# Kernel optimization log

Measured on AMD Instinct MI355X. Metric: run time of the kernel, lower is better.

## Reference

```python
import jax, jax.numpy as jnp
import numpy as np

H = 4096      # hidden_size
NH = 32       # num_heads
QR = 1536     # q_lora_rank
KVR = 512     # kv_lora_rank
RD = 64       # qk_rope_head_dim
ND = 128      # qk_nope_head_dim
VD = 128      # v_head_dim
QK = RD + ND  # qk_head_dim
EPS = 1e-6
THETA = 10000.0
B, S = 2, 1024


def rmsnorm(x, w):
    # torch: x / (||x|| * d^-0.5 + eps) * w
    norm = jnp.sqrt(jnp.sum(x * x, axis=-1, keepdims=True)) * (x.shape[-1] ** -0.5)
    return x / (norm + EPS) * w


def rope_cos_sin(seq_len):
    inv_freq = 1.0 / (THETA ** (jnp.arange(0, RD, 2, dtype=jnp.float32) / RD))
    t = jnp.arange(seq_len, dtype=jnp.float32)
    freqs = jnp.outer(t, inv_freq)              # [S, RD/2]
    emb = jnp.concatenate([freqs, freqs], -1)   # [S, RD]
    return jnp.cos(emb), jnpp_cos_sin_dummy() if False else jnp.sin(emb)


def rotate_half(x):
    x1, x2 = jnp.split(x, 2, axis=-1)
    return jnp.concatenate([-x2, x1], axis=-1)


def setup_inputs() -> dict:
    key = jax.random.key(0)
    ks = jax.random.split(key, 8)
    sc = 0.02
    return {
        "hidden_states": jax.random.normal(ks[0], (B, S, H), jnp.float32),
        "w_qa": jax.random.normal(ks[1], (H, QR), jnp.float32) * sc,
        "g_qa": jnp.ones((QR,), jnp.float32),
        "w_qb": jax.random.normal(ks[2], (QR, NH * QK), jnp.float32) * sc,
        "w_kva": jax.random.normal(ks[3], (H, KVR + RD), jnp.float32) * sc,
        "g_kva": jnp.ones((KVR,), jnp.float32),
        "w_kvb": jax.random.normal(ks[4], (KVR, NH * (ND + VD)), jnp.float32) * sc,
        "w_o": jax.random.normal(ks[5], (NH * VD, H), jnp.float32) * sc,
    }


def reference(hidden_states, w_qa, g_qa, w_qb, w_kva, g_kva, w_kvb, w_o):
    b, s, _ = hidden_states.shape
    # Q path: LoRA down -> RMSNorm -> LoRA up
    q_c = rmsnorm(hidden_states @ w_qa, g_qa)                       # [b,s,QR]
    q = (q_c @ w_qb).reshape(b, s, NH, QK).transpose(0, 2, 1, 3)    # [b,NH,s,QK]
    q_nope, q_rope = q[..., :ND], q[..., ND:]
    # KV path: joint down-proj, split compressed kv and rope key
    kv = hidden_states @ w_kva                                      # [b,s,KVR+RD]
    k_c, k_rope = kv[..., :KVR], kv[..., KVR:]
    k_c = rmsnorm(k_c, g_kva)
    kst = (k_c @ w_kvb).reshape(b, s, NH, ND + VD).transpose(0, 2, 1, 3)
    k_nope, v = kst[..., :ND], kst[..., ND:]                        # [b,NH,s,ND],[b,NH,s,VD]
    # partial RoPE on the rope slice only
    inv_freq = 1.0 / (THETA ** (jnp.arange(0, RD, 2, dtype=jnp.float32) / RD))
    freqs = jnp.outer(jnp.arange(s, dtype=jnp.float32), inv_freq)
    emb = jnp.concatenate([freqs, freqs], -1)                       # [s,RD]
    cos = jnp.cos(emb)[None, None]                                  # [1,1,s,RD]
    sin = jnp.sin(emb)[None, None]
    k_rope = k_rope[:, None]                                        # [b,1,s,RD]
    q_rope = q_rope * cos + rotate_half(q_rope) * sin
    k_rope = k_rope * cos + rotate_half(k_rope) * sin
    k_rope = jnp.broadcast_to(k_rope, (b, NH, s, RD))
    query = jnp.concatenate([q_nope, q_rope], -1)                   # [b,NH,s,QK]
    key_s = jnp.concatenate([k_nope, k_rope], -1)
    scaling = QK ** -0.5
    scores = jnp.einsum("bhqd,bhkd->bhqk", query, key_s) * scaling  # [b,NH,s,s]
    attn = jax.nn.softmax(scores, axis=-1)
    out = jnp.einsum("bhqk,bhkd->bhqd", attn, v)                    # [b,NH,s,VD]
    out = out.transpose(0, 2, 1, 3).reshape(b, s, NH * VD)
    return out @ w_o                                                # [b,s,H]
```

## Files before the change

### kernel.cpp

```cpp
#include <hip/hip_runtime.h>
#include <hip/hip_bf16.h>
#include <stdint.h>

typedef float f32x4_t __attribute__((ext_vector_type(4)));
typedef short s16x8_t __attribute__((ext_vector_type(8)));

#define LDS_AS __attribute__((address_space(3)))
#define GLB_AS __attribute__((address_space(1)))

__device__ __forceinline__ void gload16(void* lds, const void* g) {
    __builtin_amdgcn_global_load_lds((const GLB_AS uint32_t*)g,
                                     (LDS_AS uint32_t*)lds, 16, 0, 0);
}

__device__ __forceinline__ uint32_t pack_bf16(float lo, float hi) {
    union { __hip_bfloat16 h; uint16_t u; } a, b;
    a.h = __float2bfloat16(lo); b.h = __float2bfloat16(hi);
    return (uint32_t)a.u | ((uint32_t)b.u << 16);
}

__global__ __launch_bounds__(256) void rope_table_kernel(float* __restrict__ cos_t,
                                                         float* __restrict__ sin_t) {
    int idx = blockIdx.x * 256 + threadIdx.x;
    int s = idx >> 6, j = idx & 63;
    float invf = powf(10000.0f, -((float)((j & 31) * 2)) / 64.0f);
    float a = (float)s * invf;
    cos_t[idx] = cosf(a);
    sin_t[idx] = sinf(a);
}

__global__ __launch_bounds__(256) void f32_to_bf16_kernel(const float* __restrict__ in,
                                                          __hip_bfloat16* __restrict__ out, int n4) {
    int i = blockIdx.x * 256 + threadIdx.x;
    if (i >= n4) return;
    float4 v = reinterpret_cast<const float4*>(in)[i];
    struct __align__(8) BF4 { __hip_bfloat16 a, b, c, d; } r;
    r.a = __float2bfloat16(v.x); r.b = __float2bfloat16(v.y);
    r.c = __float2bfloat16(v.z); r.d = __float2bfloat16(v.w);
    reinterpret_cast<BF4*>(out)[i] = r;
}

__global__ __launch_bounds__(256) void transpose_convert(const float* __restrict__ W,
                                                         __hip_bfloat16* __restrict__ WT,
                                                         int K, int N, int Npad, float scale) {
    __shared__ float tile[32][132];
    int k0 = blockIdx.y * 32, n0 = blockIdx.x * 128;
    int tx = threadIdx.x & 31, ty = threadIdx.x >> 5;
#pragma unroll
    for (int i = 0; i < 4; i++) {
        int ky = i * 8 + ty;
        int n = n0 + tx * 4;
        float4 v;
        if (n + 3 < N) {
            v = *(const float4*)&W[(size_t)(k0 + ky) * N + n];
        } else {
            float t0 = (n + 0 < N) ? W[(size_t)(k0 + ky) * N + n + 0] : 0.f;
            float t1 = (n + 1 < N) ? W[(size_t)(k0 + ky) * N + n + 1] : 0.f;
            float t2 = (n + 2 < N) ? W[(size_t)(k0 + ky) * N + n + 2] : 0.f;
            float t3 = (n + 3 < N) ? W[(size_t)(k0 + ky) * N + n + 3] : 0.f;
            v = make_float4(t0, t1, t2, t3);
        }
        *(float4*)&tile[ky][tx * 4] = v;
    }
    __syncthreads();
    int ny = threadIdx.x & 127, kh = threadIdx.x >> 7;
#pragma unroll
    for (int oct = 0; oct < 2; oct++) {
        int kb = kh * 16 + oct * 8;
        union { short s[8]; s16x8_t v; } pk;
#pragma unroll
        for (int e = 0; e < 8; e++) {
            union { __hip_bfloat16 h; short s; } cv;
            cv.h = __float2bfloat16(tile[kb + e][ny] * scale);
            pk.s[e] = cv.s;
        }
        *(s16x8_t*)&WT[(size_t)(n0 + ny) * K + k0 + kb] = pk.v;
    }
}

__global__ __launch_bounds__(256) void rmsnorm2_kernel(const float* __restrict__ in0,
                                                       const float* __restrict__ in1,
                                                       const float* __restrict__ g,
                                                       __hip_bfloat16* __restrict__ out,
                                                       int cols, int in_stride) {
    int row = blockIdx.x;
    const float* x0 = in0 + (size_t)row * in_stride;
    const float* x1 = in1 + (size_t)row * in_stride;
    float ss = 0.f;
    for (int c = threadIdx.x; c < cols; c += 256) { float v = x0[c] + x1[c]; ss += v * v; }
#pragma unroll
    for (int off = 32; off > 0; off >>= 1) ss += __shfl_xor(ss, off);
    __shared__ float red[4];
    if ((threadIdx.x & 63) == 0) red[threadIdx.x >> 6] = ss;
    __syncthreads();
    float tot = red[0] + red[1] + red[2] + red[3];
    float rms = sqrtf(tot / (float)cols);
    float inv = 1.0f / (rms + 1e-6f);
    for (int c = threadIdx.x; c < cols; c += 256)
        out[(size_t)row * cols + c] = __float2bfloat16((x0[c] + x1[c]) * inv * g[c]);
}

__global__ __launch_bounds__(256) void rmsnorm2_rope_kernel(const float* __restrict__ in0,
                                                            const float* __restrict__ in1,
                                                            const float* __restrict__ g,
                                                            __hip_bfloat16* __restrict__ out,
                                                            const float* __restrict__ cos_t,
                                                            const float* __restrict__ sin_t,
                                                            __hip_bfloat16* __restrict__ k_rope) {
    int row = blockIdx.x;
    const float* x0 = in0 + (size_t)row * 640;
    const float* x1 = in1 + (size_t)row * 640;
    float ss = 0.f;
#pragma unroll
    for (int it = 0; it < 2; it++) {
        int c = it * 256 + threadIdx.x;
        float v = x0[c] + x1[c];
        ss += v * v;
    }
#pragma unroll
    for (int off = 32; off > 0; off >>= 1) ss += __shfl_xor(ss, off);
    __shared__ float red[4];
    if ((threadIdx.x & 63) == 0) red[threadIdx.x >> 6] = ss;
    __syncthreads();
    float tot = red[0] + red[1] + red[2] + red[3];
    float rms = sqrtf(tot / 512.0f);
    float inv = 1.0f / (rms + 1e-6f);
#pragma unroll
    for (int it = 0; it < 2; it++) {
        int c = it * 256 + threadIdx.x;
        out[(size_t)row * 512 + c] = __float2bfloat16((x0[c] + x1[c]) * inv * g[c]);
    }
    if (threadIdx.x < 32) {
        int j = threadIdx.x, s = row & 1023;
        float a1 = x0[512 + j] + x1[512 + j];
        float a2 = x0[544 + j] + x1[544 + j];
        float co = cos_t[s * 64 + j], si = sin_t[s * 64 + j];
        __hip_bfloat16* o = k_rope + (size_t)row * 64;
        o[j]      = __float2bfloat16(a1 * co - a2 * si);
        o[j + 32] = __float2bfloat16(a2 * co + a1 * si);
    }
}

template <int MODE>
__global__ __launch_bounds__(256, 3) void gemm_bt_128(const __hip_bfloat16* __restrict__ A,
                                                      const __hip_bfloat16* __restrict__ BT,
                                                      void* __restrict__ Cout, void* __restrict__ C1,
                                                      void* __restrict__ Cout2, void* __restrict__ C12,
                                                      int M, int N, int K, int Kstride, int N0, int N1,
                                                      const float* __restrict__ cos_t,
                                                      const float* __restrict__ sin_t) {
    __shared__ __hip_bfloat16 As[128 * 64];
    __shared__ __hip_bfloat16 Bs[128 * 64];
    const int tid = threadIdx.x;
    const int l = tid & 63, w = tid >> 6;
    const int wr = w >> 1, wc = w & 1;
    const int m0 = blockIdx.y * 128, n0 = blockIdx.x * 128;
    const int lrow = l & 15, lkg = l >> 4;
    const int part = (MODE == 2) ? blockIdx.z : 0;
    const int kbase = part * K;

    f32x4_t acc[4][4];
#pragma unroll
    for (int i = 0; i < 4; i++)
#pragma unroll
        for (int j = 0; j < 4; j++) acc[i][j] = (f32x4_t){0.f, 0.f, 0.f, 0.f};

    for (int k0 = 0; k0 < K; k0 += 64) {
        __syncthreads();
#pragma unroll
        for (int i = 0; i < 4; i++) {
            int s = i * 256 + tid;
            int row = s >> 3, po = s & 7;
            int lo = po ^ (row & 7);
            gload16(&As[s * 8], &A[(size_t)(m0 + row) * Kstride + kbase + k0 + lo * 8]);
            gload16(&Bs[s * 8], &BT[(size_t)(n0 + row) * Kstride + kbase + k0 + lo * 8]);
        }
        __syncthreads();
#pragma unroll
        for (int ks = 0; ks < 2; ks++) {
            s16x8_t a[4], b[4];
#pragma unroll
            for (int m = 0; m < 4; m++) {
                int row = wr * 64 + m * 16 + lrow;
                int oct = (ks * 4 + lkg) ^ (row & 7);
                a[m] = *(const s16x8_t*)&As[row * 64 + oct * 8];
            }
#pragma unroll
            for (int n = 0; n < 4; n++) {
                int row = wc * 64 + n * 16 + lrow;
                int oct = (ks * 4 + lkg) ^ (row & 7);
                b[n] = *(const s16x8_t*)&Bs[row * 64 + oct * 8];
            }
#pragma unroll
            for (int m = 0; m < 4; m++)
#pragma unroll
                for (int n = 0; n < 4; n++)
                    acc[m][n] = __builtin_amdgcn_mfma_f32_16x16x32_bf16(a[m], b[n], acc[m][n], 0, 0, 0);
        }
    }
    const bool ropeblk = (MODE == 3) && ((((n0 + wc * 64) >> 6) % 3) == 2);
    const bool vpart   = (MODE == 4) && ((((n0 + wc * 64) >> 7) & 1) != 0);
#pragma unroll
    for (int m = 0; m < 4; m++) {
        int row = m0 + wr * 64 + m * 16 + lkg * 4;
#pragma unroll
        for (int n = 0; n < 4; n++) {
            int col = n0 + wc * 64 + n * 16 + lrow;
            if (MODE == 4 && vpart) {
                int h = col >> 8, vd = (col & 255) - 128;
                int bb = row >> 10, s = row & 1023;
                uint32_t lo = pack_bf16(acc[m][n][0], acc[m][n][1]);
                uint32_t hi = pack_bf16(acc[m][n][2], acc[m][n][3]);
                uint32_t* dst = (uint32_t*)((__hip_bfloat16*)Cout2 +
                                            ((size_t)((bb * 32 + h) * 128 + vd)) * 1024 + s);
                dst[0] = lo;
                dst[1] = hi;
                continue;
            }
#pragma unroll
            for (int r = 0; r < 4; r++) {
                float v = acc[m][n][r];
                if (MODE == 3 && ropeblk) {
                    int s = (row + r) & 1023;
                    int j = ((n & 1) << 4) + lrow;
                    float co = cos_t[s * 64 + j], si = sin_t[s * 64 + j];
                    v = (n < 2) ? acc[m][n][r] * co - acc[m][n + 2][r] * si
                                : acc[m][n][r] * co + acc[m][n - 2][r] * si;
                }
                if (MODE == 1 || MODE == 3 || MODE == 4) {
                    ((__hip_bfloat16*)Cout)[(size_t)(row + r) * N + col] = __float2bfloat16(v);
                } else if (MODE == 0) {
                    ((float*)Cout)[(size_t)(row + r) * N + col] = v;
                } else {
                    float* c0 = (float*)(part ? Cout2 : Cout);
                    float* c1 = (float*)(part ? C12 : C1);
                    if (col < N0) c0[(size_t)(row + r) * N0 + col] = v;
                    else          c1[(size_t)(row + r) * N1 + (col - N0)] = v;
                }
            }
        }
    }
}

__global__ __launch_bounds__(256, 3) void attn8_kernel(const __hip_bfloat16* __restrict__ q,
                                                       const __hip_bfloat16* __restrict__ kst,
                                                       const __hip_bfloat16* __restrict__ k_rope,
                                                       const __hip_bfloat16* __restrict__ V_T,
                                                       __hip_bfloat16* __restrict__ attn_out) {
    __shared__ __align__(16) __hip_bfloat16 Ks[2][64 * 192];

    int i = blockIdx.x;
    int bh = (i & 7) * 8 + ((i >> 3) & 7);
    int qt = i >> 6;
    int h = bh & 31, b = bh >> 5;
    int q0 = qt * 64;
    int tid = threadIdx.x, l = tid & 63, w = tid >> 6;
    int lrow = l & 15, lkg = l >> 4;

    s16x8_t qa[6];
    {
        size_t qbase = (size_t)(b * 1024 + q0 + w * 16 + lrow) * 6144 + h * 192;
#pragma unroll
        for (int f = 0; f < 6; f++)
            qa[f] = *(const s16x8_t*)&q[qbase + f * 32 + lkg * 8];
    }
    f32x4_t acc_o[8];
#pragma unroll
    for (int n = 0; n < 8; n++) acc_o[n] = (f32x4_t){0.f, 0.f, 0.f, 0.f};
    float m_run = -1e30f, l_run = 0.f;

    size_t krow_base = (size_t)(b * 1024) * 8192 + h * 256;
    size_t rrow_base = (size_t)(b * 1024) * 64;
    const __hip_bfloat16* vbase = V_T + (size_t)bh * 128 * 1024 + (size_t)lrow * 1024 + lkg * 8;

    auto stage_k = [&](int kv0, int buf) {
#pragma unroll
        for (int it = 0; it < 6; it++) {
            int s = it * 256 + tid;
            int row = s / 24, po = s - row * 24;
            int lo = po ^ (row & 7);
            const __hip_bfloat16* src = (lo < 16)
                ? &kst[krow_base + (size_t)(kv0 + row) * 8192 + lo * 8]
                : &k_rope[rrow_base + (size_t)(kv0 + row) * 64 + (lo - 16) * 8];
            gload16(&Ks[buf][s * 8], src);
        }
    };

    stage_k(0, 0);
    asm volatile("s_waitcnt vmcnt(0)" ::: "memory");
    __syncthreads();

    const int src0 = lrow + ((lkg & 1) << 5);
    const int src1 = src0 + 16;
    const bool hiC = (lkg >> 1) != 0;

    int cur = 0;
    for (int kt = 0; kt < 16; kt++) {
        int kv0 = kt * 64;

        if (kt < 15) stage_k(kv0 + 64, cur ^ 1);

        f32x4_t sc[4];
#pragma unroll
        for (int c = 0; c < 4; c++) sc[c] = (f32x4_t){0.f, 0.f, 0.f, 0.f};
        __builtin_amdgcn_s_setprio(1);
#pragma unroll
        for (int c = 0; c < 4; c++) {
            int row = c * 16 + lrow;
#pragma unroll
            for (int f = 0; f < 6; f++) {
                int po = ((f * 4 + lkg) ^ (lrow & 7)) * 8;
                s16x8_t kb = *(const s16x8_t*)&Ks[cur][row * 192 + po];
                sc[c] = __builtin_amdgcn_mfma_f32_16x16x32_bf16(kb, qa[f], sc[c], 0, 0, 0);
            }
        }
        __builtin_amdgcn_s_setprio(0);

        s16x8_t vb0[8];
#pragma unroll
        for (int n = 0; n < 8; n++)
            vb0[n] = *(const s16x8_t*)&vbase[(size_t)(n * 16) * 1024 + kv0];
        __builtin_amdgcn_sched_barrier(0);

        float mx = sc[0][0];
#pragma unroll
        for (int c = 0; c < 4; c++)
#pragma unroll
            for (int r = 0; r < 4; r++) mx = fmaxf(mx, sc[c][r]);
        mx = fmaxf(mx, __shfl_xor(mx, 16));
        mx = fmaxf(mx, __shfl_xor(mx, 32));
        if (!__all(mx - m_run <= 8.0f)) {
            float mn = fmaxf(m_run, mx);
            float al = __expf(m_run - mn);
            m_run = mn;
            l_run *= al;
#pragma unroll
            for (int n = 0; n < 8; n++) acc_o[n] *= al;
        }
        uint32_t u[4][2];
        float sum = 0.f;
#pragma unroll
        for (int c = 0; c < 4; c++) {
            float p0 = __expf(sc[c][0] - m_run), p1 = __expf(sc[c][1] - m_run);
            float p2 = __expf(sc[c][2] - m_run), p3 = __expf(sc[c][3] - m_run);
            sum += (p0 + p1) + (p2 + p3);
            u[c][0] = pack_bf16(p0, p1);
            u[c][1] = pack_bf16(p2, p3);
        }
        sum += __shfl_xor(sum, 16);
        sum += __shfl_xor(sum, 32);
        l_run += sum;

        {
            uint32_t a0 = __shfl((int)u[0][0], src0), b0 = __shfl((int)u[1][0], src0);
            uint32_t a1 = __shfl((int)u[0][1], src0), b1 = __shfl((int)u[1][1], src0);
            uint32_t a2 = __shfl((int)u[0][0], src1), b2 = __shfl((int)u[1][0], src1);
            uint32_t a3 = __shfl((int)u[0][1], src1), b3 = __shfl((int)u[1][1], src1);
            union { uint32_t wd[4]; s16x8_t v; } pb;
            pb.wd[0] = hiC ? b0 : a0;
            pb.wd[1] = hiC ? b1 : a1;
            pb.wd[2] = hiC ? b2 : a2;
            pb.wd[3] = hiC ? b3 : a3;
            __builtin_amdgcn_s_setprio(1);
#pragma unroll
            for (int n = 0; n < 8; n++)
                acc_o[n] = __builtin_amdgcn_mfma_f32_16x16x32_bf16(vb0[n], pb.v, acc_o[n], 0, 0, 0);
            __builtin_amdgcn_s_setprio(0);
        }
        s16x8_t vb1[8];
#pragma unroll
        for (int n = 0; n < 8; n++)
            vb1[n] = *(const s16x8_t*)&vbase[(size_t)(n * 16) * 1024 + kv0 + 32];
        {
            uint32_t a0 = __shfl((int)u[2][0], src0), b0 = __shfl((int)u[3][0], src0);
            uint32_t a1 = __shfl((int)u[2][1], src0), b1 = __shfl((int)u[3][1], src0);
            uint32_t a2 = __shfl((int)u[2][0], src1), b2 = __shfl((int)u[3][0], src1);
            uint32_t a3 = __shfl((int)u[2][1], src1), b3 = __shfl((int)u[3][1], src1);
            union { uint32_t wd[4]; s16x8_t v; } pb;
            pb.wd[0] = hiC ? b0 : a0;
            pb.wd[1] = hiC ? b1 : a1;
            pb.wd[2] = hiC ? b2 : a2;
            pb.wd[3] = hiC ? b3 : a3;
            __builtin_amdgcn_s_setprio(1);
#pragma unroll
            for (int n = 0; n < 8; n++)
                acc_o[n] = __builtin_amdgcn_mfma_f32_16x16x32_bf16(vb1[n], pb.v, acc_o[n], 0, 0, 0);
            __builtin_amdgcn_s_setprio(0);
        }

        asm volatile("s_waitcnt vmcnt(0)" ::: "memory");
        __syncthreads();
        cur ^= 1;
    }

    float inv = 1.0f / l_run;
    __hip_bfloat16* Ob = &Ks[0][0] + (size_t)w * (16 * 136);
#pragma unroll
    for (int n = 0; n < 8; n++) {
        uint32_t lo = pack_bf16(acc_o[n][0] * inv, acc_o[n][1] * inv);
        uint32_t hi = pack_bf16(acc_o[n][2] * inv, acc_o[n][3] * inv);
        uint32_t* dst = (uint32_t*)&Ob[lrow * 136 + n * 16 + lkg * 4];
        dst[0] = lo;
        dst[1] = hi;
    }
    asm volatile("s_waitcnt lgkmcnt(0)" ::: "memory");
    __builtin_amdgcn_sched_barrier(0);
#pragma unroll
    for (int it = 0; it < 4; it++) {
        int tr = it * 4 + lkg;
        s16x8_t ov = *(const s16x8_t*)&Ob[tr * 136 + lrow * 8];
        *(s16x8_t*)&attn_out[(size_t)(b * 1024 + q0 + w * 16 + tr) * 4096 + h * 128 + lrow * 8] = ov;
    }
}

extern "C" void kernel_launch(void* const* d_in, const int* in_sizes, int n_in,
                              void* d_out, int out_size, void* d_ws, size_t ws_size,
                              hipStream_t stream) {
    const float* hidden = (const float*)d_in[0];
    const float* w_qa   = (const float*)d_in[1];
    const float* g_qa   = (const float*)d_in[2];
    const float* w_qb   = (const float*)d_in[3];
    const float* w_kva  = (const float*)d_in[4];
    const float* g_kva  = (const float*)d_in[5];
    const float* w_kvb  = (const float*)d_in[6];
    const float* w_o    = (const float*)d_in[7];
    float* out = (float*)d_out;

    char* base = (char*)d_ws;
    size_t off = 0;
    auto alloc = [&](size_t bytes) -> void* {
        off = (off + 255) & ~(size_t)255;
        void* p = base + off;
        off += bytes;
        return p;
    };
    float* cos_t = (float*)alloc(1024 * 64 * 4);
    float* sin_t = (float*)alloc(1024 * 64 * 4);
    __hip_bfloat16* hid_b  = (__hip_bfloat16*)alloc(2048ull * 4096 * 2);
    __hip_bfloat16* wqaT   = (__hip_bfloat16*)alloc(1536ull * 4096 * 2);
    __hip_bfloat16* wkvaT  = (__hip_bfloat16*)alloc(640ull * 4096 * 2);
    __hip_bfloat16* wqbT   = (__hip_bfloat16*)alloc(6144ull * 1536 * 2);
    __hip_bfloat16* wkvbT  = (__hip_bfloat16*)alloc(8192ull * 512 * 2);
    __hip_bfloat16* woT    = (__hip_bfloat16*)alloc(4096ull * 4096 * 2);
    float* q_a             = (float*)alloc(2048ull * 1536 * 4);
    __hip_bfloat16* q_c    = (__hip_bfloat16*)alloc(2048ull * 1536 * 2);
    __hip_bfloat16* q_buf  = (__hip_bfloat16*)alloc(2048ull * 6144 * 2);
    float* kv              = (float*)alloc(2048ull * 640 * 4);
    __hip_bfloat16* k_c    = (__hip_bfloat16*)alloc(2048ull * 512 * 2);
    __hip_bfloat16* k_rope = (__hip_bfloat16*)alloc(2048ull * 64 * 2);
    __hip_bfloat16* kst    = (__hip_bfloat16*)alloc(2048ull * 8192 * 2);
    __hip_bfloat16* V_T      = hid_b;
    __hip_bfloat16* attn_out = wqbT;
    float* q_a1 = (float*)q_buf;
    float* kv1  = (float*)((char*)q_buf + 2048ull * 1536 * 4);

    const float qscale = 0.07216878364870323f;

    rope_table_kernel<<<256, 256, 0, stream>>>(cos_t, sin_t);
    f32_to_bf16_kernel<<<8192, 256, 0, stream>>>(hidden, hid_b, 2048 * 4096 / 4);
    transpose_convert<<<dim3(1536 / 128, 4096 / 32), 256, 0, stream>>>(w_qa, wqaT, 4096, 1536, 1536, 1.0f);
    transpose_convert<<<dim3(640 / 128, 4096 / 32), 256, 0, stream>>>(w_kva, wkvaT, 4096, 576, 640, 1.0f);
    transpose_convert<<<dim3(6144 / 128, 1536 / 32), 256, 0, stream>>>(w_qb, wqbT, 1536, 6144, 6144, qscale);
    transpose_convert<<<dim3(8192 / 128, 512 / 32), 256, 0, stream>>>(w_kvb, wkvbT, 512, 8192, 8192, 1.0f);
    transpose_convert<<<dim3(4096 / 128, 4096 / 32), 256, 0, stream>>>(w_o, woT, 4096, 4096, 4096, 1.0f);

    gemm_bt_128<2><<<dim3(17, 16, 2), 256, 0, stream>>>(hid_b, wqaT, q_a, kv, q_a1, kv1,
                                                        2048, 2176, 2048, 4096, 1536, 640,
                                                        nullptr, nullptr);
    rmsnorm2_kernel<<<2048, 256, 0, stream>>>(q_a, q_a1, g_qa, q_c, 1536, 1536);
    rmsnorm2_rope_kernel<<<2048, 256, 0, stream>>>(kv, kv1, g_kva, k_c, cos_t, sin_t, k_rope);
    gemm_bt_128<3><<<dim3(6144 / 128, 16), 256, 0, stream>>>(q_c, wqbT, q_buf, nullptr, nullptr, nullptr,
                                                             2048, 6144, 1536, 1536, 0, 0, cos_t, sin_t);
    gemm_bt_128<4><<<dim3(8192 / 128, 16), 256, 0, stream>>>(k_c, wkvbT, kst, nullptr, V_T, nullptr,
                                                             2048, 8192, 512, 512, 0, 0, nullptr, nullptr);
    attn8_kernel<<<1024, 256, 0, stream>>>(q_buf, kst, k_rope, V_T, attn_out);
    gemm_bt_128<0><<<dim3(4096 / 128, 16), 256, 0, stream>>>(attn_out, woT, out, nullptr, nullptr, nullptr,
                                                             2048, 4096, 4096, 4096, 0, 0, nullptr, nullptr);
}
```

Baseline: 442.5 us.

## Load shared rope keys directly into registers and defer row-sum reduction

```diff
diff --git a/kernel.cpp b/kernel.cpp
--- a/kernel.cpp
+++ b/kernel.cpp
@@ -242,12 +242,12 @@
     }
 }
 
-__global__ __launch_bounds__(256, 3) void attn8_kernel(const __hip_bfloat16* __restrict__ q,
-                                                       const __hip_bfloat16* __restrict__ kst,
-                                                       const __hip_bfloat16* __restrict__ k_rope,
-                                                       const __hip_bfloat16* __restrict__ V_T,
-                                                       __hip_bfloat16* __restrict__ attn_out) {
-    __shared__ __align__(16) __hip_bfloat16 Ks[2][64 * 192];
+__global__ __launch_bounds__(256, 3) void attn13_kernel(const __hip_bfloat16* __restrict__ q,
+                                                        const __hip_bfloat16* __restrict__ kst,
+                                                        const __hip_bfloat16* __restrict__ k_rope,
+                                                        const __hip_bfloat16* __restrict__ V_T,
+                                                        __hip_bfloat16* __restrict__ attn_out) {
+    __shared__ __align__(16) __hip_bfloat16 Ks[2][64 * 128];
 
     int i = blockIdx.x;
     int bh = (i & 7) * 8 + ((i >> 3) & 7);
@@ -267,26 +267,23 @@
     f32x4_t acc_o[8];
 #pragma unroll
     for (int n = 0; n < 8; n++) acc_o[n] = (f32x4_t){0.f, 0.f, 0.f, 0.f};
-    float m_run = -1e30f, l_run = 0.f;
+    float m_run = -1e30f, l_part = 0.f;
 
     size_t krow_base = (size_t)(b * 1024) * 8192 + h * 256;
     size_t rrow_base = (size_t)(b * 1024) * 64;
     const __hip_bfloat16* vbase = V_T + (size_t)bh * 128 * 1024 + (size_t)lrow * 1024 + lkg * 8;
 
-    auto stage_k = [&](int kv0, int buf) {
-#pragma unroll
-        for (int it = 0; it < 6; it++) {
+    auto stage_nope = [&](int kvs, int buf) {
+#pragma unroll
+        for (int it = 0; it < 4; it++) {
             int s = it * 256 + tid;
-            int row = s / 24, po = s - row * 24;
+            int row = s >> 4, po = s & 15;
             int lo = po ^ (row & 7);
-            const __hip_bfloat16* src = (lo < 16)
-                ? &kst[krow_base + (size_t)(kv0 + row) * 8192 + lo * 8]
-                : &k_rope[rrow_base + (size_t)(kv0 + row) * 64 + (lo - 16) * 8];
-            gload16(&Ks[buf][s * 8], src);
+            gload16(&Ks[buf][s * 8], &kst[krow_base + (size_t)(kvs + row) * 8192 + lo * 8]);
         }
     };
 
-    stage_k(0, 0);
+    stage_nope(0, 0);
     asm volatile("s_waitcnt vmcnt(0)" ::: "memory");
     __syncthreads();
 
@@ -298,7 +295,15 @@
     for (int kt = 0; kt < 16; kt++) {
         int kv0 = kt * 64;
 
-        if (kt < 15) stage_k(kv0 + 64, cur ^ 1);
+        s16x8_t kr[4][2];
+#pragma unroll
+        for (int c = 0; c < 4; c++)
+#pragma unroll
+            for (int f = 0; f < 2; f++)
+                kr[c][f] = *(const s16x8_t*)&k_rope[rrow_base +
+                               (size_t)(kv0 + c * 16 + lrow) * 64 + f * 32 + lkg * 8];
+        if (kt < 15) stage_nope(kv0 + 64, cur ^ 1);
+        __builtin_amdgcn_sched_barrier(0);
 
         f32x4_t sc[4];
 #pragma unroll
@@ -308,11 +313,16 @@
         for (int c = 0; c < 4; c++) {
             int row = c * 16 + lrow;
 #pragma unroll
-            for (int f = 0; f < 6; f++) {
-                int po = ((f * 4 + lkg) ^ (lrow & 7)) * 8;
-                s16x8_t kb = *(const s16x8_t*)&Ks[cur][row * 192 + po];
+            for (int f = 0; f < 4; f++) {
+                int po = ((f * 4 + lkg) ^ (row & 7)) * 8;
+                s16x8_t kb = *(const s16x8_t*)&Ks[cur][row * 128 + po];
                 sc[c] = __builtin_amdgcn_mfma_f32_16x16x32_bf16(kb, qa[f], sc[c], 0, 0, 0);
             }
+        }
+#pragma unroll
+        for (int c = 0; c < 4; c++) {
+            sc[c] = __builtin_amdgcn_mfma_f32_16x16x32_bf16(kr[c][0], qa[4], sc[c], 0, 0, 0);
+            sc[c] = __builtin_amdgcn_mfma_f32_16x16x32_bf16(kr[c][1], qa[5], sc[c], 0, 0, 0);
         }
         __builtin_amdgcn_s_setprio(0);
 
@@ -333,23 +343,19 @@
             float mn = fmaxf(m_run, mx);
             float al = __expf(m_run - mn);
             m_run = mn;
-            l_run *= al;
+            l_part *= al;
 #pragma unroll
             for (int n = 0; n < 8; n++) acc_o[n] *= al;
         }
         uint32_t u[4][2];
-        float sum = 0.f;
 #pragma unroll
         for (int c = 0; c < 4; c++) {
             float p0 = __expf(sc[c][0] - m_run), p1 = __expf(sc[c][1] - m_run);
             float p2 = __expf(sc[c][2] - m_run), p3 = __expf(sc[c][3] - m_run);
-            sum += (p0 + p1) + (p2 + p3);
+            l_part += (p0 + p1) + (p2 + p3);
             u[c][0] = pack_bf16(p0, p1);
             u[c][1] = pack_bf16(p2, p3);
         }
-        sum += __shfl_xor(sum, 16);
-        sum += __shfl_xor(sum, 32);
-        l_run += sum;
 
         {
             uint32_t a0 = __shfl((int)u[0][0], src0), b0 = __shfl((int)u[1][0], src0);
@@ -393,7 +399,10 @@
         cur ^= 1;
     }
 
-    float inv = 1.0f / l_run;
+    float lsum = l_part;
+    lsum += __shfl_xor(lsum, 16);
+    lsum += __shfl_xor(lsum, 32);
+    float inv = 1.0f / lsum;
     __hip_bfloat16* Ob = &Ks[0][0] + (size_t)w * (16 * 136);
 #pragma unroll
     for (int n = 0; n < 8; n++) {
@@ -473,7 +482,7 @@
                                                              2048, 6144, 1536, 1536, 0, 0, cos_t, sin_t);
     gemm_bt_128<4><<<dim3(8192 / 128, 16), 256, 0, stream>>>(k_c, wkvbT, kst, nullptr, V_T, nullptr,
                                                              2048, 8192, 512, 512, 0, 0, nullptr, nullptr);
-    attn8_kernel<<<1024, 256, 0, stream>>>(q_buf, kst, k_rope, V_T, attn_out);
+    attn13_kernel<<<1024, 256, 0, stream>>>(q_buf, kst, k_rope, V_T, attn_out);
     gemm_bt_128<0><<<dim3(4096 / 128, 16), 256, 0, stream>>>(attn_out, woT, out, nullptr, nullptr, nullptr,
                                                              2048, 4096, 4096, 4096, 0, 0, nullptr, nullptr);
 }
```

Result: slower. 486.0 us (+9.8%).
